# Optimization experiments

Measured on AMD Instinct MI355X. Metric: run time of the kernel, lower is better.

The kernel has to match this reference:

```python
import jax, jax.numpy as jnp
import numpy as np

N = 50000
F_IN = 256
H1, D1 = 8, 8            # conv1: 8 heads x 8 dims, concat -> 64
H2, C = 8, 16            # conv2: 8 heads x num_classes, concat -> 128
NEG_SLOPE = 0.2


def setup_inputs() -> dict:
    key = jax.random.key(0)
    ks = jax.random.split(key, 10)
    x = jax.random.normal(ks[0], (N, F_IN), dtype=jnp.float32)
    edge_index = jax.random.randint(ks[1], (2, 800000), 0, N, dtype=jnp.int64)
    s1 = 1.0 / np.sqrt(F_IN)
    s2 = 1.0 / np.sqrt(H1 * D1)
    return {
        "x": x,
        "edge_index": edge_index,
        "W1": jax.random.normal(ks[2], (F_IN, H1 * D1), dtype=jnp.float32) * s1,
        "a1_src": jax.random.normal(ks[3], (H1, D1), dtype=jnp.float32) * s2,
        "a1_dst": jax.random.normal(ks[4], (H1, D1), dtype=jnp.float32) * s2,
        "b1": jnp.zeros((H1 * D1,), dtype=jnp.float32),
        "W2": jax.random.normal(ks[5], (H1 * D1, H2 * C), dtype=jnp.float32) * s2,
        "a2_src": jax.random.normal(ks[6], (H2, C), dtype=jnp.float32) * (1.0 / np.sqrt(C)),
        "a2_dst": jax.random.normal(ks[7], (H2, C), dtype=jnp.float32) * (1.0 / np.sqrt(C)),
        "b2": jnp.zeros((H2 * C,), dtype=jnp.float32),
    }


def _add_self_loops(edge_index, n):
    loops = jnp.arange(n, dtype=edge_index.dtype)
    return jnp.concatenate([edge_index, jnp.stack([loops, loops])], axis=1)


def _gat_conv(x, src, dst, W, a_src, a_dst, b, heads, out_dim, n):
    # xw: [N, H, O]
    xw = (x @ W).reshape(n, heads, out_dim)
    al_src = jnp.einsum("nho,ho->nh", xw, a_src)  # [N, H]
    al_dst = jnp.einsum("nho,ho->nh", xw, a_dst)
    e = jax.nn.leaky_relu(al_src[src] + al_dst[dst], NEG_SLOPE)  # [E, H]
    # segment softmax over edges sharing a destination node
    e_max = jax.ops.segment_max(e, dst, num_segments=n)
    e_exp = jnp.exp(e - e_max[dst])
    denom = jax.ops.segment_sum(e_exp, dst, num_segments=n)
    alpha = e_exp / (denom[dst] + 1e-16)                          # [E, H]
    msg = xw[src] * alpha[:, :, None]                              # [E, H, O]
    out = jax.ops.segment_sum(msg, dst, num_segments=n)           # [N, H, O]
    return out.reshape(n, heads * out_dim) + b, alpha


def reference(x, edge_index, W1, a1_src, a1_dst, b1, W2, a2_src, a2_dst, b2):
    ei = _add_self_loops(edge_index, N)
    src, dst = ei[0], ei[1]
    # dropout is a no-op at inference (training=False)
    h1, alpha1 = _gat_conv(x, src, dst, W1, a1_src, a1_dst, b1, H1, D1, N)
    h1 = jax.nn.elu(h1)
    h2, _ = _gat_conv(h1, src, dst, W2, a2_src, a2_dst, b2, H2, C, N)
    logp = jax.nn.log_softmax(h2, axis=1)
    return logp, alpha1
```

## Files before the change

kernel.cpp:

```cpp
#include <hip/hip_runtime.h>

#define N_NODES 50000
#define N_EDGES 800000
#define N_TOT   850000
#define NEG 0.2f
#define ELLW 64

#define G1_TILES 391
#define G2_TILES 782

__device__ __forceinline__ float leaky(float x) { return x > 0.f ? x : NEG * x; }

__device__ __forceinline__ unsigned bf16pk(float a, float b) {
  unsigned ua = __float_as_uint(a), ub = __float_as_uint(b);
  ua = (ua + 0x7FFFu + ((ua >> 16) & 1u)) >> 16;
  ub = (ub + 0x7FFFu + ((ub >> 16) & 1u)) >> 16;
  return ua | (ub << 16);
}
__device__ __forceinline__ float blo(unsigned u) { return __uint_as_float(u << 16); }
__device__ __forceinline__ float bhi(unsigned u) { return __uint_as_float(u & 0xFFFF0000u); }
__device__ __forceinline__ float bh2f(unsigned short h) { return __uint_as_float(((unsigned)h) << 16); }

__global__ __launch_bounds__(256) void gemm1_ell_k(const float* __restrict__ x,
    const float* __restrict__ W1, const float* __restrict__ a1sv, const float* __restrict__ a1dv,
    unsigned short* __restrict__ xw1h, float* __restrict__ al1s, float* __restrict__ al1d,
    const int* __restrict__ srcA, const int* __restrict__ dstA,
    int* __restrict__ cnt, int* __restrict__ ell)
{
  __shared__ float xs[32 * 128];
  __shared__ float wsm[32 * 64];
  if (blockIdx.x >= G1_TILES) {
    int e = (blockIdx.x - G1_TILES) * 256 + threadIdx.x;
    if (e < N_EDGES) {
      int d = dstA[e], s = srcA[e];
      int p = atomicAdd(&cnt[d], 1);
      if (p < ELLW) ell[d * ELLW + p] = s;
    }
    return;
  }
  const int t = threadIdx.x;
  const int tx = t & 15, ty = t >> 4;
  const int n0 = blockIdx.x * 128;
  const int nl = t >> 1;
  const int ks = (t & 1) * 16;
  const int wk = t >> 3;
  const int wc = (t & 7) * 8;
  int gn = n0 + nl; if (gn >= N_NODES) gn = N_NODES - 1;
  const float* xrowb = x + (size_t)gn * 256 + ks;

  float acc[8][4];
#pragma unroll
  for (int r = 0; r < 8; ++r)
#pragma unroll
    for (int i = 0; i < 4; ++i) acc[r][i] = 0.f;

  for (int kc = 0; kc < 8; ++kc) {
    const int kb = kc * 32;
    const float4* xp = (const float4*)(xrowb + kb);
    float4 v0 = xp[0], v1 = xp[1], v2 = xp[2], v3 = xp[3];
    const float* wrow = W1 + (size_t)(kb + wk) * 64 + wc;
    float4 w0 = ((const float4*)wrow)[0];
    float4 w1 = ((const float4*)wrow)[1];
    __syncthreads();
    xs[(ks + 0) * 128 + nl] = v0.x;  xs[(ks + 1) * 128 + nl] = v0.y;
    xs[(ks + 2) * 128 + nl] = v0.z;  xs[(ks + 3) * 128 + nl] = v0.w;
    xs[(ks + 4) * 128 + nl] = v1.x;  xs[(ks + 5) * 128 + nl] = v1.y;
    xs[(ks + 6) * 128 + nl] = v1.z;  xs[(ks + 7) * 128 + nl] = v1.w;
    xs[(ks + 8) * 128 + nl] = v2.x;  xs[(ks + 9) * 128 + nl] = v2.y;
    xs[(ks + 10) * 128 + nl] = v2.z; xs[(ks + 11) * 128 + nl] = v2.w;
    xs[(ks + 12) * 128 + nl] = v3.x; xs[(ks + 13) * 128 + nl] = v3.y;
    xs[(ks + 14) * 128 + nl] = v3.z; xs[(ks + 15) * 128 + nl] = v3.w;
    ((float4*)&wsm[wk * 64 + wc])[0] = w0;
    ((float4*)&wsm[wk * 64 + wc])[1] = w1;
    __syncthreads();
#pragma unroll 4
    for (int k = 0; k < 32; ++k) {
      float4 xa = *(const float4*)&xs[k * 128 + ty * 8];
      float4 xb = *(const float4*)&xs[k * 128 + ty * 8 + 4];
      float4 wv = *(const float4*)&wsm[k * 64 + tx * 4];
      float xn[8]; *(float4*)&xn[0] = xa; *(float4*)&xn[4] = xb;
      float wn[4]; *(float4*)wn = wv;
#pragma unroll
      for (int r = 0; r < 8; ++r)
#pragma unroll
        for (int i = 0; i < 4; ++i) acc[r][i] += xn[r] * wn[i];
    }
  }
  float cs[4], cd[4];
#pragma unroll
  for (int i = 0; i < 4; ++i) { cs[i] = a1sv[tx * 4 + i]; cd[i] = a1dv[tx * 4 + i]; }
#pragma unroll
  for (int r = 0; r < 8; ++r) {
    int n = n0 + ty * 8 + r;
    if (n >= N_NODES) break;
    uint2 pk;
    pk.x = bf16pk(acc[r][0], acc[r][1]);
    pk.y = bf16pk(acc[r][2], acc[r][3]);
    *(uint2*)(xw1h + (size_t)n * 64 + tx * 4) = pk;
    float ps = acc[r][0] * cs[0] + acc[r][1] * cs[1] + acc[r][2] * cs[2] + acc[r][3] * cs[3];
    float pd = acc[r][0] * cd[0] + acc[r][1] * cd[1] + acc[r][2] * cd[2] + acc[r][3] * cd[3];
    ps += __shfl_xor(ps, 1);
    pd += __shfl_xor(pd, 1);
    if ((tx & 1) == 0) {
      al1s[n * 8 + (tx >> 1)] = ps;
      al1d[n * 8 + (tx >> 1)] = pd;
    }
  }
}

__global__ __launch_bounds__(256) void agg1_k(const unsigned short* __restrict__ xw1h,
    const float* __restrict__ al1s, const float* __restrict__ al1d,
    const int* __restrict__ cnt, const int* __restrict__ ell,
    const float* __restrict__ b1, float* __restrict__ h1, float* __restrict__ denom1)
{
  const int lane = threadIdx.x & 63;
  const int n = blockIdx.x * 4 + (threadIdx.x >> 6);
  if (n >= N_NODES) return;
  const int h = lane >> 3;
  const float ad = al1d[n * 8 + h];
  float ws = __expf(leaky(al1s[n * 8 + h] + ad));
  float den0 = ws, den1r = 0.f;
  float acc0 = ws * bh2f(xw1h[(size_t)n * 64 + lane]), acc1 = 0.f;
  int num = cnt[n]; if (num > ELLW) num = ELLW;
  const int4* cp = (const int4*)(ell + (size_t)n * ELLW);
  int i = 0;
  for (; i + 8 <= num; i += 8) {
    int4 A = cp[i >> 2], B = cp[(i >> 2) + 1];
    float l0 = al1s[A.x * 8 + h] + ad, l1 = al1s[A.y * 8 + h] + ad;
    float l2 = al1s[A.z * 8 + h] + ad, l3 = al1s[A.w * 8 + h] + ad;
    float l4 = al1s[B.x * 8 + h] + ad, l5 = al1s[B.y * 8 + h] + ad;
    float l6 = al1s[B.z * 8 + h] + ad, l7 = al1s[B.w * 8 + h] + ad;
    float v0 = bh2f(xw1h[(size_t)A.x * 64 + lane]), v1 = bh2f(xw1h[(size_t)A.y * 64 + lane]);
    float v2 = bh2f(xw1h[(size_t)A.z * 64 + lane]), v3 = bh2f(xw1h[(size_t)A.w * 64 + lane]);
    float v4 = bh2f(xw1h[(size_t)B.x * 64 + lane]), v5 = bh2f(xw1h[(size_t)B.y * 64 + lane]);
    float v6 = bh2f(xw1h[(size_t)B.z * 64 + lane]), v7 = bh2f(xw1h[(size_t)B.w * 64 + lane]);
    float w0 = __expf(leaky(l0)), w1 = __expf(leaky(l1));
    float w2 = __expf(leaky(l2)), w3 = __expf(leaky(l3));
    float w4 = __expf(leaky(l4)), w5 = __expf(leaky(l5));
    float w6 = __expf(leaky(l6)), w7 = __expf(leaky(l7));
    acc0 += w0 * v0; acc1 += w1 * v1; acc0 += w2 * v2; acc1 += w3 * v3;
    acc0 += w4 * v4; acc1 += w5 * v5; acc0 += w6 * v6; acc1 += w7 * v7;
    den0 += w0 + w2 + w4 + w6; den1r += w1 + w3 + w5 + w7;
  }
  for (; i + 4 <= num; i += 4) {
    int4 A = cp[i >> 2];
    float l0 = al1s[A.x * 8 + h] + ad, l1 = al1s[A.y * 8 + h] + ad;
    float l2 = al1s[A.z * 8 + h] + ad, l3 = al1s[A.w * 8 + h] + ad;
    float v0 = bh2f(xw1h[(size_t)A.x * 64 + lane]), v1 = bh2f(xw1h[(size_t)A.y * 64 + lane]);
    float v2 = bh2f(xw1h[(size_t)A.z * 64 + lane]), v3 = bh2f(xw1h[(size_t)A.w * 64 + lane]);
    float w0 = __expf(leaky(l0)), w1 = __expf(leaky(l1));
    float w2 = __expf(leaky(l2)), w3 = __expf(leaky(l3));
    acc0 += w0 * v0; acc1 += w1 * v1; acc0 += w2 * v2; acc1 += w3 * v3;
    den0 += w0 + w2; den1r += w1 + w3;
  }
  for (; i < num; ++i) {
    int s = ell[(size_t)n * ELLW + i];
    float w = __expf(leaky(al1s[s * 8 + h] + ad));
    acc0 += w * bh2f(xw1h[(size_t)s * 64 + lane]);
    den0 += w;
  }
  float den = den0 + den1r, acc = acc0 + acc1;
  if ((lane & 7) == 0) denom1[n * 8 + h] = den;
  float o = acc / (den + 1e-16f) + b1[lane];
  h1[(size_t)n * 64 + lane] = o > 0.f ? o : (__expf(o) - 1.f);
}

__global__ __launch_bounds__(256) void gemm2_alpha_k(const float* __restrict__ h1,
    const float* __restrict__ W2, const float* __restrict__ a2sv, const float* __restrict__ a2dv,
    unsigned* __restrict__ xw2b, float* __restrict__ al2s, float* __restrict__ al2d,
    const int* __restrict__ srcA, const int* __restrict__ dstA,
    const float* __restrict__ al1s, const float* __restrict__ al1d,
    const float* __restrict__ denom1, float* __restrict__ alpha_out)
{
  __shared__ float xs[64 * 64];
  __shared__ float wsm[64 * 128];
  if (blockIdx.x >= G2_TILES) {
    int e = (blockIdx.x - G2_TILES) * 256 + threadIdx.x;
    if (e >= N_TOT) return;
    int s, d;
    if (e < N_EDGES) { s = srcA[e]; d = dstA[e]; }
    else             { s = d = e - N_EDGES; }
    float4 as0 = ((const float4*)(al1s + s * 8))[0];
    float4 as1 = ((const float4*)(al1s + s * 8))[1];
    float4 ad0 = ((const float4*)(al1d + d * 8))[0];
    float4 ad1 = ((const float4*)(al1d + d * 8))[1];
    float4 dn0 = ((const float4*)(denom1 + d * 8))[0];
    float4 dn1 = ((const float4*)(denom1 + d * 8))[1];
    float4 o0, o1;
    o0.x = __expf(leaky(as0.x + ad0.x)) / (dn0.x + 1e-16f);
    o0.y = __expf(leaky(as0.y + ad0.y)) / (dn0.y + 1e-16f);
    o0.z = __expf(leaky(as0.z + ad0.z)) / (dn0.z + 1e-16f);
    o0.w = __expf(leaky(as0.w + ad0.w)) / (dn0.w + 1e-16f);
    o1.x = __expf(leaky(as1.x + ad1.x)) / (dn1.x + 1e-16f);
    o1.y = __expf(leaky(as1.y + ad1.y)) / (dn1.y + 1e-16f);
    o1.z = __expf(leaky(as1.z + ad1.z)) / (dn1.z + 1e-16f);
    o1.w = __expf(leaky(as1.w + ad1.w)) / (dn1.w + 1e-16f);
    ((float4*)(alpha_out + (size_t)e * 8))[0] = o0;
    ((float4*)(alpha_out + (size_t)e * 8))[1] = o1;
    return;
  }
  const int t = threadIdx.x;
  const int tx = t & 15, ty = t >> 4;
  const int n0 = blockIdx.x * 64;
  {
    const int nl = t >> 2;
    const int ks = (t & 3) * 16;
    int gn = n0 + nl; if (gn >= N_NODES) gn = N_NODES - 1;
    const float4* hp = (const float4*)(h1 + (size_t)gn * 64 + ks);
#pragma unroll
    for (int j = 0; j < 4; ++j) {
      float4 v = hp[j];
      xs[(ks + 4 * j + 0) * 64 + nl] = v.x;
      xs[(ks + 4 * j + 1) * 64 + nl] = v.y;
      xs[(ks + 4 * j + 2) * 64 + nl] = v.z;
      xs[(ks + 4 * j + 3) * 64 + nl] = v.w;
    }
    const int wk = t >> 2;
    const int wc = (t & 3) * 32;
    const float4* wp = (const float4*)(W2 + (size_t)wk * 128 + wc);
    float4* wd = (float4*)&wsm[wk * 128 + wc];
#pragma unroll
    for (int j = 0; j < 8; ++j) wd[j] = wp[j];
  }
  __syncthreads();
  float acc[4][8];
#pragma unroll
  for (int r = 0; r < 4; ++r)
#pragma unroll
    for (int i = 0; i < 8; ++i) acc[r][i] = 0.f;
#pragma unroll 4
  for (int k = 0; k < 64; ++k) {
    float4 xa = *(const float4*)&xs[k * 64 + ty * 4];
    float4 wa = *(const float4*)&wsm[k * 128 + tx * 8];
    float4 wb = *(const float4*)&wsm[k * 128 + tx * 8 + 4];
    float xn[4]; *(float4*)xn = xa;
    float wn[8]; *(float4*)&wn[0] = wa; *(float4*)&wn[4] = wb;
#pragma unroll
    for (int r = 0; r < 4; ++r)
#pragma unroll
      for (int i = 0; i < 8; ++i) acc[r][i] += xn[r] * wn[i];
  }
  float cs[8], cd[8];
#pragma unroll
  for (int i = 0; i < 8; ++i) { cs[i] = a2sv[tx * 8 + i]; cd[i] = a2dv[tx * 8 + i]; }
#pragma unroll
  for (int r = 0; r < 4; ++r) {
    int n = n0 + ty * 4 + r;
    if (n >= N_NODES) break;
    uint4 pk;
    pk.x = bf16pk(acc[r][0], acc[r][1]);
    pk.y = bf16pk(acc[r][2], acc[r][3]);
    pk.z = bf16pk(acc[r][4], acc[r][5]);
    pk.w = bf16pk(acc[r][6], acc[r][7]);
    *(uint4*)(xw2b + (size_t)n * 64 + tx * 4) = pk;
    float ps = 0.f, pd = 0.f;
#pragma unroll
    for (int i = 0; i < 8; ++i) { ps += acc[r][i] * cs[i]; pd += acc[r][i] * cd[i]; }
    ps += __shfl_xor(ps, 1);
    pd += __shfl_xor(pd, 1);
    if ((tx & 1) == 0) {
      al2s[n * 8 + (tx >> 1)] = ps;
      al2d[n * 8 + (tx >> 1)] = pd;
    }
  }
}

__global__ __launch_bounds__(256) void agg2_k(const unsigned* __restrict__ xw2b,
    const float* __restrict__ al2s, const float* __restrict__ al2d,
    const int* __restrict__ cnt, const int* __restrict__ ell,
    const float* __restrict__ b2, float* __restrict__ logp)
{
  const int lane = threadIdx.x & 63;
  const int n = blockIdx.x * 4 + (threadIdx.x >> 6);
  if (n >= N_NODES) return;
  const int h = lane >> 3;
  const float ad = al2d[n * 8 + h];
  float ws = __expf(leaky(al2s[n * 8 + h] + ad));
  unsigned su = xw2b[(size_t)n * 64 + lane];
  float den0 = ws, den1r = 0.f;
  float ax0 = ws * blo(su), ay0 = ws * bhi(su), ax1 = 0.f, ay1 = 0.f;
  int num = cnt[n]; if (num > ELLW) num = ELLW;
  const int4* cp = (const int4*)(ell + (size_t)n * ELLW);
  int i = 0;
  for (; i + 8 <= num; i += 8) {
    int4 A = cp[i >> 2], B = cp[(i >> 2) + 1];
    float l0 = al2s[A.x * 8 + h] + ad, l1 = al2s[A.y * 8 + h] + ad;
    float l2 = al2s[A.z * 8 + h] + ad, l3 = al2s[A.w * 8 + h] + ad;
    float l4 = al2s[B.x * 8 + h] + ad, l5 = al2s[B.y * 8 + h] + ad;
    float l6 = al2s[B.z * 8 + h] + ad, l7 = al2s[B.w * 8 + h] + ad;
    unsigned u0 = xw2b[(size_t)A.x * 64 + lane], u1 = xw2b[(size_t)A.y * 64 + lane];
    unsigned u2 = xw2b[(size_t)A.z * 64 + lane], u3 = xw2b[(size_t)A.w * 64 + lane];
    unsigned u4 = xw2b[(size_t)B.x * 64 + lane], u5 = xw2b[(size_t)B.y * 64 + lane];
    unsigned u6 = xw2b[(size_t)B.z * 64 + lane], u7 = xw2b[(size_t)B.w * 64 + lane];
    float w0 = __expf(leaky(l0)), w1 = __expf(leaky(l1));
    float w2 = __expf(leaky(l2)), w3 = __expf(leaky(l3));
    float w4 = __expf(leaky(l4)), w5 = __expf(leaky(l5));
    float w6 = __expf(leaky(l6)), w7 = __expf(leaky(l7));
    ax0 += w0 * blo(u0); ay0 += w0 * bhi(u0);
    ax1 += w1 * blo(u1); ay1 += w1 * bhi(u1);
    ax0 += w2 * blo(u2); ay0 += w2 * bhi(u2);
    ax1 += w3 * blo(u3); ay1 += w3 * bhi(u3);
    ax0 += w4 * blo(u4); ay0 += w4 * bhi(u4);
    ax1 += w5 * blo(u5); ay1 += w5 * bhi(u5);
    ax0 += w6 * blo(u6); ay0 += w6 * bhi(u6);
    ax1 += w7 * blo(u7); ay1 += w7 * bhi(u7);
    den0 += w0 + w2 + w4 + w6; den1r += w1 + w3 + w5 + w7;
  }
  for (; i + 4 <= num; i += 4) {
    int4 A = cp[i >> 2];
    float l0 = al2s[A.x * 8 + h] + ad, l1 = al2s[A.y * 8 + h] + ad;
    float l2 = al2s[A.z * 8 + h] + ad, l3 = al2s[A.w * 8 + h] + ad;
    unsigned u0 = xw2b[(size_t)A.x * 64 + lane], u1 = xw2b[(size_t)A.y * 64 + lane];
    unsigned u2 = xw2b[(size_t)A.z * 64 + lane], u3 = xw2b[(size_t)A.w * 64 + lane];
    float w0 = __expf(leaky(l0)), w1 = __expf(leaky(l1));
    float w2 = __expf(leaky(l2)), w3 = __expf(leaky(l3));
    ax0 += w0 * blo(u0); ay0 += w0 * bhi(u0);
    ax1 += w1 * blo(u1); ay1 += w1 * bhi(u1);
    ax0 += w2 * blo(u2); ay0 += w2 * bhi(u2);
    ax1 += w3 * blo(u3); ay1 += w3 * bhi(u3);
    den0 += w0 + w2; den1r += w1 + w3;
  }
  for (; i < num; ++i) {
    int s = ell[(size_t)n * ELLW + i];
    float w = __expf(leaky(al2s[s * 8 + h] + ad));
    unsigned u = xw2b[(size_t)s * 64 + lane];
    ax0 += w * blo(u); ay0 += w * bhi(u); den0 += w;
  }
  float inv = 1.f / (den0 + den1r + 1e-16f);
  float o0 = (ax0 + ax1) * inv + b2[2 * lane];
  float o1 = (ay0 + ay1) * inv + b2[2 * lane + 1];
  float mx = fmaxf(o0, o1);
#pragma unroll
  for (int off = 1; off < 64; off <<= 1) mx = fmaxf(mx, __shfl_xor(mx, off));
  float se = __expf(o0 - mx) + __expf(o1 - mx);
#pragma unroll
  for (int off = 1; off < 64; off <<= 1) se += __shfl_xor(se, off);
  float lse = mx + __logf(se);
  float2 o; o.x = o0 - lse; o.y = o1 - lse;
  ((float2*)logp)[(size_t)n * 64 + lane] = o;
}

extern "C" void kernel_launch(void* const* d_in, const int* in_sizes, int n_in,
                              void* d_out, int out_size, void* d_ws, size_t ws_size,
                              hipStream_t stream)
{
  const float* x   = (const float*)d_in[0];
  const int*   ei  = (const int*)d_in[1];
  const float* W1  = (const float*)d_in[2];
  const float* a1s = (const float*)d_in[3];
  const float* a1d = (const float*)d_in[4];
  const float* b1  = (const float*)d_in[5];
  const float* W2  = (const float*)d_in[6];
  const float* a2s = (const float*)d_in[7];
  const float* a2d = (const float*)d_in[8];
  const float* b2  = (const float*)d_in[9];
  const int* srcA = ei;
  const int* dstA = ei + N_EDGES;

  char* ws = (char*)d_ws;
  unsigned short* xw1h = (unsigned short*)ws;            ws += (size_t)N_NODES * 64 * 2;
  float* h1    = (float*)ws;  ws += (size_t)N_NODES * 64 * 4;
  unsigned* xw2b = (unsigned*)ws; ws += (size_t)N_NODES * 64 * 4;
  float* al1s_ = (float*)ws;  ws += (size_t)N_NODES * 8 * 4;
  float* al1d_ = (float*)ws;  ws += (size_t)N_NODES * 8 * 4;
  float* den1_ = (float*)ws;  ws += (size_t)N_NODES * 8 * 4;
  float* al2s_ = (float*)ws;  ws += (size_t)N_NODES * 8 * 4;
  float* al2d_ = (float*)ws;  ws += (size_t)N_NODES * 8 * 4;
  int* cnt    = (int*)ws;     ws += (size_t)N_NODES * 4;
  int* ell    = (int*)ws;     ws += (size_t)N_NODES * ELLW * 4;

  float* logp      = (float*)d_out;
  float* alpha_out = logp + (size_t)N_NODES * 128;

  hipMemsetAsync(cnt, 0, N_NODES * sizeof(int), stream);

  gemm1_ell_k<<<G1_TILES + (N_EDGES + 255) / 256, 256, 0, stream>>>(
      x, W1, a1s, a1d, xw1h, al1s_, al1d_, srcA, dstA, cnt, ell);
  agg1_k<<<(N_NODES + 3) / 4, 256, 0, stream>>>(xw1h, al1s_, al1d_, cnt, ell, b1, h1, den1_);
  gemm2_alpha_k<<<G2_TILES + (N_TOT + 255) / 256, 256, 0, stream>>>(
      h1, W2, a2s, a2d, xw2b, al2s_, al2d_, srcA, dstA, al1s_, al1d_, den1_, alpha_out);
  agg2_k<<<(N_NODES + 3) / 4, 256, 0, stream>>>(xw2b, al2s_, al2d_, cnt, ell, b2, logp);
}
```

Baseline: 177.6 us.

## Use split-bf16 MFMA for layer-1 GEMM with folded attention projections and 16-bit ELL

Replaces the FP32 SIMT tiled GEMM for x@W1 with a 16x16x32 bf16 MFMA path. Each operand is split into hi/lo bf16 parts and three MFMAs are issued to keep near-fp32 accuracy. The attention projections W1·a_src and W1·a_dst are precomputed into LDS as an extra 16-column fragment, so the alpha logits come out of the same MFMA pass. The ELL adjacency now stores source indices as 16-bit values, which is valid only because N is below 65536, and the edge-insertion blocks read four edges per thread with vector loads. This halves index traffic in both aggregation kernels, at the cost of extra split conversions and triple MFMA work.

```diff
diff --git a/kernel.cpp b/kernel.cpp
--- a/kernel.cpp
+++ b/kernel.cpp
@@ -7,7 +7,11 @@
 #define ELLW 64
 
 #define G1_TILES 391
+#define EB1      782
 #define G2_TILES 782
+
+typedef __attribute__((ext_vector_type(8))) short bf16x8;
+typedef __attribute__((ext_vector_type(4))) float f32x4;
 
 __device__ __forceinline__ float leaky(float x) { return x > 0.f ? x : NEG * x; }
 
@@ -21,96 +25,133 @@
 __device__ __forceinline__ float bhi(unsigned u) { return __uint_as_float(u & 0xFFFF0000u); }
 __device__ __forceinline__ float bh2f(unsigned short h) { return __uint_as_float(((unsigned)h) << 16); }
 
+__device__ __forceinline__ unsigned cvtpk(float a, float b) {
+  unsigned r; asm("v_cvt_pk_bf16_f32 %0, %1, %2" : "=v"(r) : "v"(a), "v"(b)); return r;
+}
+__device__ __forceinline__ bf16x8 asbf(uint4 u) { union { uint4 a; bf16x8 b; } c; c.a = u; return c.b; }
+
+__device__ __forceinline__ void split8(const float* v, uint4& hi, uint4& lo) {
+  unsigned h[4], lw[4];
+#pragma unroll
+  for (int p = 0; p < 4; ++p) {
+    float a = v[2 * p], b = v[2 * p + 1];
+    unsigned hp = cvtpk(a, b);
+    float ra = a - __uint_as_float(hp << 16);
+    float rb = b - __uint_as_float(hp & 0xFFFF0000u);
+    h[p] = hp;
+    lw[p] = cvtpk(ra, rb);
+  }
+  hi = make_uint4(h[0], h[1], h[2], h[3]);
+  lo = make_uint4(lw[0], lw[1], lw[2], lw[3]);
+}
+
 __global__ __launch_bounds__(256) void gemm1_ell_k(const float* __restrict__ x,
     const float* __restrict__ W1, const float* __restrict__ a1sv, const float* __restrict__ a1dv,
     unsigned short* __restrict__ xw1h, float* __restrict__ al1s, float* __restrict__ al1d,
     const int* __restrict__ srcA, const int* __restrict__ dstA,
-    int* __restrict__ cnt, int* __restrict__ ell)
+    int* __restrict__ cnt, unsigned short* __restrict__ ell)
 {
-  __shared__ float xs[32 * 128];
-  __shared__ float wsm[32 * 64];
-  if (blockIdx.x >= G1_TILES) {
-    int e = (blockIdx.x - G1_TILES) * 256 + threadIdx.x;
-    if (e < N_EDGES) {
-      int d = dstA[e], s = srcA[e];
-      int p = atomicAdd(&cnt[d], 1);
-      if (p < ELLW) ell[d * ELLW + p] = s;
+  __shared__ float pl[256][17];
+  if (blockIdx.x < EB1) {
+    int q = blockIdx.x * 256 + threadIdx.x;
+    if (q * 4 < N_EDGES) {
+      int4 dv = ((const int4*)dstA)[q];
+      int4 sv = ((const int4*)srcA)[q];
+      int p;
+      p = atomicAdd(&cnt[dv.x], 1); if (p < ELLW) ell[dv.x * ELLW + p] = (unsigned short)sv.x;
+      p = atomicAdd(&cnt[dv.y], 1); if (p < ELLW) ell[dv.y * ELLW + p] = (unsigned short)sv.y;
+      p = atomicAdd(&cnt[dv.z], 1); if (p < ELLW) ell[dv.z * ELLW + p] = (unsigned short)sv.z;
+      p = atomicAdd(&cnt[dv.w], 1); if (p < ELLW) ell[dv.w * ELLW + p] = (unsigned short)sv.w;
     }
     return;
   }
   const int t = threadIdx.x;
-  const int tx = t & 15, ty = t >> 4;
-  const int n0 = blockIdx.x * 128;
-  const int nl = t >> 1;
-  const int ks = (t & 1) * 16;
-  const int wk = t >> 3;
-  const int wc = (t & 7) * 8;
-  int gn = n0 + nl; if (gn >= N_NODES) gn = N_NODES - 1;
-  const float* xrowb = x + (size_t)gn * 256 + ks;
-
-  float acc[8][4];
-#pragma unroll
-  for (int r = 0; r < 8; ++r)
-#pragma unroll
-    for (int i = 0; i < 4; ++i) acc[r][i] = 0.f;
-
-  for (int kc = 0; kc < 8; ++kc) {
-    const int kb = kc * 32;
-    const float4* xp = (const float4*)(xrowb + kb);
-    float4 v0 = xp[0], v1 = xp[1], v2 = xp[2], v3 = xp[3];
-    const float* wrow = W1 + (size_t)(kb + wk) * 64 + wc;
-    float4 w0 = ((const float4*)wrow)[0];
-    float4 w1 = ((const float4*)wrow)[1];
-    __syncthreads();
-    xs[(ks + 0) * 128 + nl] = v0.x;  xs[(ks + 1) * 128 + nl] = v0.y;
-    xs[(ks + 2) * 128 + nl] = v0.z;  xs[(ks + 3) * 128 + nl] = v0.w;
-    xs[(ks + 4) * 128 + nl] = v1.x;  xs[(ks + 5) * 128 + nl] = v1.y;
-    xs[(ks + 6) * 128 + nl] = v1.z;  xs[(ks + 7) * 128 + nl] = v1.w;
-    xs[(ks + 8) * 128 + nl] = v2.x;  xs[(ks + 9) * 128 + nl] = v2.y;
-    xs[(ks + 10) * 128 + nl] = v2.z; xs[(ks + 11) * 128 + nl] = v2.w;
-    xs[(ks + 12) * 128 + nl] = v3.x; xs[(ks + 13) * 128 + nl] = v3.y;
-    xs[(ks + 14) * 128 + nl] = v3.z; xs[(ks + 15) * 128 + nl] = v3.w;
-    ((float4*)&wsm[wk * 64 + wc])[0] = w0;
-    ((float4*)&wsm[wk * 64 + wc])[1] = w1;
-    __syncthreads();
-#pragma unroll 4
-    for (int k = 0; k < 32; ++k) {
-      float4 xa = *(const float4*)&xs[k * 128 + ty * 8];
-      float4 xb = *(const float4*)&xs[k * 128 + ty * 8 + 4];
-      float4 wv = *(const float4*)&wsm[k * 64 + tx * 4];
-      float xn[8]; *(float4*)&xn[0] = xa; *(float4*)&xn[4] = xb;
-      float wn[4]; *(float4*)wn = wv;
-#pragma unroll
-      for (int r = 0; r < 8; ++r)
-#pragma unroll
-        for (int i = 0; i < 4; ++i) acc[r][i] += xn[r] * wn[i];
-    }
-  }
-  float cs[4], cd[4];
-#pragma unroll
-  for (int i = 0; i < 4; ++i) { cs[i] = a1sv[tx * 4 + i]; cd[i] = a1dv[tx * 4 + i]; }
-#pragma unroll
-  for (int r = 0; r < 8; ++r) {
-    int n = n0 + ty * 8 + r;
-    if (n >= N_NODES) break;
-    uint2 pk;
-    pk.x = bf16pk(acc[r][0], acc[r][1]);
-    pk.y = bf16pk(acc[r][2], acc[r][3]);
-    *(uint2*)(xw1h + (size_t)n * 64 + tx * 4) = pk;
-    float ps = acc[r][0] * cs[0] + acc[r][1] * cs[1] + acc[r][2] * cs[2] + acc[r][3] * cs[3];
-    float pd = acc[r][0] * cd[0] + acc[r][1] * cd[1] + acc[r][2] * cd[2] + acc[r][3] * cd[3];
-    ps += __shfl_xor(ps, 1);
-    pd += __shfl_xor(pd, 1);
-    if ((tx & 1) == 0) {
-      al1s[n * 8 + (tx >> 1)] = ps;
-      al1d[n * 8 + (tx >> 1)] = pd;
-    }
-  }
+  {
+    const float* wr = W1 + t * 64;
+    float po[16];
+#pragma unroll
+    for (int j = 0; j < 16; ++j) po[j] = 0.f;
+#pragma unroll
+    for (int o = 0; o < 64; ++o) {
+      float wv = wr[o];
+      po[o >> 3]       += wv * a1sv[o];
+      po[8 + (o >> 3)] += wv * a1dv[o];
+    }
+#pragma unroll
+    for (int j = 0; j < 16; ++j) pl[t][j] = po[j];
+  }
+  __syncthreads();
+
+  const int w = t >> 6, l = t & 63;
+  const int lr = l & 15, lk = l >> 4;
+  const int n0 = (blockIdx.x - EB1) * 128 + w * 32;
+  int r0 = n0 + lr;      if (r0 > N_NODES - 1) r0 = N_NODES - 1;
+  int r1 = n0 + 16 + lr; if (r1 > N_NODES - 1) r1 = N_NODES - 1;
+  const float* xp0 = x + (size_t)r0 * 256 + lk * 8;
+  const float* xp1 = x + (size_t)r1 * 256 + lk * 8;
+
+  f32x4 acc[2][5];
+#pragma unroll
+  for (int a = 0; a < 2; ++a)
+#pragma unroll
+    for (int b = 0; b < 5; ++b) acc[a][b] = (f32x4){0.f, 0.f, 0.f, 0.f};
+
+  for (int kb = 0; kb < 256; kb += 32) {
+    uint4 bh[5], bl[5];
+#pragma unroll
+    for (int cf = 0; cf < 4; ++cf) {
+      const float* wp = W1 + (size_t)(kb + lk * 8) * 64 + cf * 16 + lr;
+      float bv[8];
+#pragma unroll
+      for (int j = 0; j < 8; ++j) bv[j] = wp[(size_t)j * 64];
+      split8(bv, bh[cf], bl[cf]);
+    }
+    {
+      float pv[8];
+#pragma unroll
+      for (int j = 0; j < 8; ++j) pv[j] = pl[kb + lk * 8 + j][lr];
+      split8(pv, bh[4], bl[4]);
+    }
+    float av[8];
+    uint4 ah, am;
+    *(float4*)&av[0] = *(const float4*)(xp0 + kb);
+    *(float4*)&av[4] = *(const float4*)(xp0 + kb + 4);
+    split8(av, ah, am);
+#pragma unroll
+    for (int cf = 0; cf < 5; ++cf) {
+      acc[0][cf] = __builtin_amdgcn_mfma_f32_16x16x32_bf16(asbf(ah), asbf(bh[cf]), acc[0][cf], 0, 0, 0);
+      acc[0][cf] = __builtin_amdgcn_mfma_f32_16x16x32_bf16(asbf(am), asbf(bh[cf]), acc[0][cf], 0, 0, 0);
+      acc[0][cf] = __builtin_amdgcn_mfma_f32_16x16x32_bf16(asbf(ah), asbf(bl[cf]), acc[0][cf], 0, 0, 0);
+    }
+    *(float4*)&av[0] = *(const float4*)(xp1 + kb);
+    *(float4*)&av[4] = *(const float4*)(xp1 + kb + 4);
+    split8(av, ah, am);
+#pragma unroll
+    for (int cf = 0; cf < 5; ++cf) {
+      acc[1][cf] = __builtin_amdgcn_mfma_f32_16x16x32_bf16(asbf(ah), asbf(bh[cf]), acc[1][cf], 0, 0, 0);
+      acc[1][cf] = __builtin_amdgcn_mfma_f32_16x16x32_bf16(asbf(am), asbf(bh[cf]), acc[1][cf], 0, 0, 0);
+      acc[1][cf] = __builtin_amdgcn_mfma_f32_16x16x32_bf16(asbf(ah), asbf(bl[cf]), acc[1][cf], 0, 0, 0);
+    }
+  }
+#pragma unroll
+  for (int rf = 0; rf < 2; ++rf)
+#pragma unroll
+    for (int r = 0; r < 4; ++r) {
+      int n = n0 + rf * 16 + lk * 4 + r;
+      if (n < N_NODES) {
+#pragma unroll
+        for (int cf = 0; cf < 4; ++cf)
+          xw1h[(size_t)n * 64 + cf * 16 + lr] = (unsigned short)bf16pk(acc[rf][cf][r], 0.f);
+        float av_ = acc[rf][4][r];
+        if (lr < 8) al1s[n * 8 + lr] = av_;
+        else        al1d[n * 8 + lr - 8] = av_;
+      }
+    }
 }
 
 __global__ __launch_bounds__(256) void agg1_k(const unsigned short* __restrict__ xw1h,
     const float* __restrict__ al1s, const float* __restrict__ al1d,
-    const int* __restrict__ cnt, const int* __restrict__ ell,
+    const int* __restrict__ cnt, const unsigned short* __restrict__ ell,
     const float* __restrict__ b1, float* __restrict__ h1, float* __restrict__ denom1)
 {
   const int lane = threadIdx.x & 63;
@@ -122,18 +163,22 @@
   float den0 = ws, den1r = 0.f;
   float acc0 = ws * bh2f(xw1h[(size_t)n * 64 + lane]), acc1 = 0.f;
   int num = cnt[n]; if (num > ELLW) num = ELLW;
-  const int4* cp = (const int4*)(ell + (size_t)n * ELLW);
+  const uint4* cp = (const uint4*)(ell + (size_t)n * ELLW);
   int i = 0;
   for (; i + 8 <= num; i += 8) {
-    int4 A = cp[i >> 2], B = cp[(i >> 2) + 1];
-    float l0 = al1s[A.x * 8 + h] + ad, l1 = al1s[A.y * 8 + h] + ad;
-    float l2 = al1s[A.z * 8 + h] + ad, l3 = al1s[A.w * 8 + h] + ad;
-    float l4 = al1s[B.x * 8 + h] + ad, l5 = al1s[B.y * 8 + h] + ad;
-    float l6 = al1s[B.z * 8 + h] + ad, l7 = al1s[B.w * 8 + h] + ad;
-    float v0 = bh2f(xw1h[(size_t)A.x * 64 + lane]), v1 = bh2f(xw1h[(size_t)A.y * 64 + lane]);
-    float v2 = bh2f(xw1h[(size_t)A.z * 64 + lane]), v3 = bh2f(xw1h[(size_t)A.w * 64 + lane]);
-    float v4 = bh2f(xw1h[(size_t)B.x * 64 + lane]), v5 = bh2f(xw1h[(size_t)B.y * 64 + lane]);
-    float v6 = bh2f(xw1h[(size_t)B.z * 64 + lane]), v7 = bh2f(xw1h[(size_t)B.w * 64 + lane]);
+    uint4 A = cp[i >> 3];
+    int s0 = A.x & 0xFFFF, s1 = (int)(A.x >> 16);
+    int s2 = A.y & 0xFFFF, s3 = (int)(A.y >> 16);
+    int s4 = A.z & 0xFFFF, s5 = (int)(A.z >> 16);
+    int s6 = A.w & 0xFFFF, s7 = (int)(A.w >> 16);
+    float l0 = al1s[s0 * 8 + h] + ad, l1 = al1s[s1 * 8 + h] + ad;
+    float l2 = al1s[s2 * 8 + h] + ad, l3 = al1s[s3 * 8 + h] + ad;
+    float l4 = al1s[s4 * 8 + h] + ad, l5 = al1s[s5 * 8 + h] + ad;
+    float l6 = al1s[s6 * 8 + h] + ad, l7 = al1s[s7 * 8 + h] + ad;
+    float v0 = bh2f(xw1h[(size_t)s0 * 64 + lane]), v1 = bh2f(xw1h[(size_t)s1 * 64 + lane]);
+    float v2 = bh2f(xw1h[(size_t)s2 * 64 + lane]), v3 = bh2f(xw1h[(size_t)s3 * 64 + lane]);
+    float v4 = bh2f(xw1h[(size_t)s4 * 64 + lane]), v5 = bh2f(xw1h[(size_t)s5 * 64 + lane]);
+    float v6 = bh2f(xw1h[(size_t)s6 * 64 + lane]), v7 = bh2f(xw1h[(size_t)s7 * 64 + lane]);
     float w0 = __expf(leaky(l0)), w1 = __expf(leaky(l1));
     float w2 = __expf(leaky(l2)), w3 = __expf(leaky(l3));
     float w4 = __expf(leaky(l4)), w5 = __expf(leaky(l5));
@@ -143,11 +188,13 @@
     den0 += w0 + w2 + w4 + w6; den1r += w1 + w3 + w5 + w7;
   }
   for (; i + 4 <= num; i += 4) {
-    int4 A = cp[i >> 2];
-    float l0 = al1s[A.x * 8 + h] + ad, l1 = al1s[A.y * 8 + h] + ad;
-    float l2 = al1s[A.z * 8 + h] + ad, l3 = al1s[A.w * 8 + h] + ad;
-    float v0 = bh2f(xw1h[(size_t)A.x * 64 + lane]), v1 = bh2f(xw1h[(size_t)A.y * 64 + lane]);
-    float v2 = bh2f(xw1h[(size_t)A.z * 64 + lane]), v3 = bh2f(xw1h[(size_t)A.w * 64 + lane]);
+    uint2 A = *(const uint2*)(ell + (size_t)n * ELLW + i);
+    int s0 = A.x & 0xFFFF, s1 = (int)(A.x >> 16);
+    int s2 = A.y & 0xFFFF, s3 = (int)(A.y >> 16);
+    float l0 = al1s[s0 * 8 + h] + ad, l1 = al1s[s1 * 8 + h] + ad;
+    float l2 = al1s[s2 * 8 + h] + ad, l3 = al1s[s3 * 8 + h] + ad;
+    float v0 = bh2f(xw1h[(size_t)s0 * 64 + lane]), v1 = bh2f(xw1h[(size_t)s1 * 64 + lane]);
+    float v2 = bh2f(xw1h[(size_t)s2 * 64 + lane]), v3 = bh2f(xw1h[(size_t)s3 * 64 + lane]);
     float w0 = __expf(leaky(l0)), w1 = __expf(leaky(l1));
     float w2 = __expf(leaky(l2)), w3 = __expf(leaky(l3));
     acc0 += w0 * v0; acc1 += w1 * v1; acc0 += w2 * v2; acc1 += w3 * v3;
@@ -267,7 +314,7 @@
 
 __global__ __launch_bounds__(256) void agg2_k(const unsigned* __restrict__ xw2b,
     const float* __restrict__ al2s, const float* __restrict__ al2d,
-    const int* __restrict__ cnt, const int* __restrict__ ell,
+    const int* __restrict__ cnt, const unsigned short* __restrict__ ell,
     const float* __restrict__ b2, float* __restrict__ logp)
 {
   const int lane = threadIdx.x & 63;
@@ -280,18 +327,22 @@
   float den0 = ws, den1r = 0.f;
   float ax0 = ws * blo(su), ay0 = ws * bhi(su), ax1 = 0.f, ay1 = 0.f;
   int num = cnt[n]; if (num > ELLW) num = ELLW;
-  const int4* cp = (const int4*)(ell + (size_t)n * ELLW);
+  const uint4* cp = (const uint4*)(ell + (size_t)n * ELLW);
   int i = 0;
   for (; i + 8 <= num; i += 8) {
-    int4 A = cp[i >> 2], B = cp[(i >> 2) + 1];
-    float l0 = al2s[A.x * 8 + h] + ad, l1 = al2s[A.y * 8 + h] + ad;
-    float l2 = al2s[A.z * 8 + h] + ad, l3 = al2s[A.w * 8 + h] + ad;
-    float l4 = al2s[B.x * 8 + h] + ad, l5 = al2s[B.y * 8 + h] + ad;
-    float l6 = al2s[B.z * 8 + h] + ad, l7 = al2s[B.w * 8 + h] + ad;
-    unsigned u0 = xw2b[(size_t)A.x * 64 + lane], u1 = xw2b[(size_t)A.y * 64 + lane];
-    unsigned u2 = xw2b[(size_t)A.z * 64 + lane], u3 = xw2b[(size_t)A.w * 64 + lane];
-    unsigned u4 = xw2b[(size_t)B.x * 64 + lane], u5 = xw2b[(size_t)B.y * 64 + lane];
-    unsigned u6 = xw2b[(size_t)B.z * 64 + lane], u7 = xw2b[(size_t)B.w * 64 + lane];
+    uint4 A = cp[i >> 3];
+    int s0 = A.x & 0xFFFF, s1 = (int)(A.x >> 16);
+    int s2 = A.y & 0xFFFF, s3 = (int)(A.y >> 16);
+    int s4 = A.z & 0xFFFF, s5 = (int)(A.z >> 16);
+    int s6 = A.w & 0xFFFF, s7 = (int)(A.w >> 16);
+    float l0 = al2s[s0 * 8 + h] + ad, l1 = al2s[s1 * 8 + h] + ad;
+    float l2 = al2s[s2 * 8 + h] + ad, l3 = al2s[s3 * 8 + h] + ad;
+    float l4 = al2s[s4 * 8 + h] + ad, l5 = al2s[s5 * 8 + h] + ad;
+    float l6 = al2s[s6 * 8 + h] + ad, l7 = al2s[s7 * 8 + h] + ad;
+    unsigned u0 = xw2b[(size_t)s0 * 64 + lane], u1 = xw2b[(size_t)s1 * 64 + lane];
+    unsigned u2 = xw2b[(size_t)s2 * 64 + lane], u3 = xw2b[(size_t)s3 * 64 + lane];
+    unsigned u4 = xw2b[(size_t)s4 * 64 + lane], u5 = xw2b[(size_t)s5 * 64 + lane];
+    unsigned u6 = xw2b[(size_t)s6 * 64 + lane], u7 = xw2b[(size_t)s7 * 64 + lane];
     float w0 = __expf(leaky(l0)), w1 = __expf(leaky(l1));
     float w2 = __expf(leaky(l2)), w3 = __expf(leaky(l3));
     float w4 = __expf(leaky(l4)), w5 = __expf(leaky(l5));
@@ -307,11 +358,13 @@
     den0 += w0 + w2 + w4 + w6; den1r += w1 + w3 + w5 + w7;
   }
   for (; i + 4 <= num; i += 4) {
-    int4 A = cp[i >> 2];
-    float l0 = al2s[A.x * 8 + h] + ad, l1 = al2s[A.y * 8 + h] + ad;
-    float l2 = al2s[A.z * 8 + h] + ad, l3 = al2s[A.w * 8 + h] + ad;
-    unsigned u0 = xw2b[(size_t)A.x * 64 + lane], u1 = xw2b[(size_t)A.y * 64 + lane];
-    unsigned u2 = xw2b[(size_t)A.z * 64 + lane], u3 = xw2b[(size_t)A.w * 64 + lane];
+    uint2 A = *(const uint2*)(ell + (size_t)n * ELLW + i);
+    int s0 = A.x & 0xFFFF, s1 = (int)(A.x >> 16);
+    int s2 = A.y & 0xFFFF, s3 = (int)(A.y >> 16);
+    float l0 = al2s[s0 * 8 + h] + ad, l1 = al2s[s1 * 8 + h] + ad;
+    float l2 = al2s[s2 * 8 + h] + ad, l3 = al2s[s3 * 8 + h] + ad;
+    unsigned u0 = xw2b[(size_t)s0 * 64 + lane], u1 = xw2b[(size_t)s1 * 64 + lane];
+    unsigned u2 = xw2b[(size_t)s2 * 64 + lane], u3 = xw2b[(size_t)s3 * 64 + lane];
     float w0 = __expf(leaky(l0)), w1 = __expf(leaky(l1));
     float w2 = __expf(leaky(l2)), w3 = __expf(leaky(l3));
     ax0 += w0 * blo(u0); ay0 += w0 * bhi(u0);
@@ -367,14 +420,14 @@
   float* al2s_ = (float*)ws;  ws += (size_t)N_NODES * 8 * 4;
   float* al2d_ = (float*)ws;  ws += (size_t)N_NODES * 8 * 4;
   int* cnt    = (int*)ws;     ws += (size_t)N_NODES * 4;
-  int* ell    = (int*)ws;     ws += (size_t)N_NODES * ELLW * 4;
+  unsigned short* ell = (unsigned short*)ws; ws += (size_t)N_NODES * ELLW * 2;
 
   float* logp      = (float*)d_out;
   float* alpha_out = logp + (size_t)N_NODES * 128;
 
   hipMemsetAsync(cnt, 0, N_NODES * sizeof(int), stream);
 
-  gemm1_ell_k<<<G1_TILES + (N_EDGES + 255) / 256, 256, 0, stream>>>(
+  gemm1_ell_k<<<EB1 + G1_TILES, 256, 0, stream>>>(
       x, W1, a1s, a1d, xw1h, al1s_, al1d_, srcA, dstA, cnt, ell);
   agg1_k<<<(N_NODES + 3) / 4, 256, 0, stream>>>(xw1h, al1s_, al1d_, cnt, ell, b1, h1, den1_);
   gemm2_alpha_k<<<G2_TILES + (N_TOT + 255) / 256, 256, 0, stream>>>(
```

Result: slower. 197.9 us (+11.4%).
